# Performance work log

Hardware: AMD Instinct MI355X
Metric: run time of the kernel (lower is better)

Reference implementation:

```python
import jax, jax.numpy as jnp
import numpy as np

N_NODES = 100000
N_EDGES = 1600000
IN_FEATS = 128
N_HIDDEN = 128
N_CLASSES = 16
INIT_EPS = 0.0
N_GIN_LAYERS = 4  # n_layers + 1


def setup_inputs() -> dict:
    key = jax.random.key(0)
    ks = jax.random.split(key, 16)
    features = jax.random.normal(ks[0], (N_NODES, IN_FEATS), dtype=jnp.float32)
    src = jax.random.randint(ks[1], (N_EDGES,), 0, N_NODES, dtype=jnp.int64)
    dst = jax.random.randint(ks[2], (N_EDGES,), 0, N_NODES, dtype=jnp.int64)
    def linear(k, fin, fout):
        bound = 1.0 / np.sqrt(fin)
        kw, kb = jax.random.split(k)
        W = jax.random.uniform(kw, (fin, fout), jnp.float32, -bound, bound)
        b = jax.random.uniform(kb, (fout,), jnp.float32, -bound, bound)
        return W, b
    W0, b0 = linear(ks[3], IN_FEATS, N_HIDDEN)
    W1, b1 = linear(ks[4], N_HIDDEN, N_HIDDEN)
    W2, b2 = linear(ks[5], N_HIDDEN, N_HIDDEN)
    W3, b3 = linear(ks[6], N_HIDDEN, N_CLASSES)
    eps = jnp.full((N_GIN_LAYERS,), INIT_EPS, dtype=jnp.float32)
    return {"features": features, "src": src, "dst": dst,
            "W0": W0, "b0": b0, "W1": W1, "b1": b1,
            "W2": W2, "b2": b2, "W3": W3, "b3": b3, "eps": eps}


def _mean_agg(h, src, dst, inv_deg):
    # gather neighbor features along edges, sum into dst, divide by in-degree
    agg = jax.ops.segment_sum(h[src], dst, num_segments=N_NODES)
    return agg * inv_deg


def _gin_layer(h, src, dst, inv_deg, eps, W, b, relu):
    z = (1.0 + eps) * h + _mean_agg(h, src, dst, inv_deg)
    out = z @ W + b  # Dropout is identity in eval mode
    return jax.nn.relu(out) if relu else out


def reference(features, src, dst, W0, b0, W1, b1, W2, b2, W3, b3, eps):
    deg = jax.ops.segment_sum(jnp.ones((src.shape[0],), features.dtype), dst,
                              num_segments=N_NODES)
    inv_deg = (1.0 / jnp.maximum(deg, 1.0))[:, None]
    h = _gin_layer(features, src, dst, inv_deg, eps[0], W0, b0, relu=True)
    h = _gin_layer(h, src, dst, inv_deg, eps[1], W1, b1, relu=True)
    h = _gin_layer(h, src, dst, inv_deg, eps[2], W2, b2, relu=True)
    h = _gin_layer(h, src, dst, inv_deg, eps[3], W3, b3, relu=False)
    return h
```

## Files before the change

### kernel.cpp

```cpp
#include <hip/hip_runtime.h>

#define NODES 100000
#define EDGES 1600000
#define FEATS 128
#define NCLS  16

#define BSH    6
#define BNODES 64
#define NB     ((NODES + BNODES - 1) / BNODES)
#define CHUNK  8192
#define NBLK   ((EDGES + CHUNK - 1) / CHUNK)
#define NHIST  (NB * NBLK)
#define BCAP   2048
#define NGRP   ((NODES + 15) / 16)

typedef unsigned int  u32;
typedef unsigned short u16;
typedef unsigned long long u64;
typedef __attribute__((ext_vector_type(8))) short short8;
typedef __attribute__((ext_vector_type(4))) float f32x4;

__device__ __forceinline__ float b2f(u16 v){ return __uint_as_float(((u32)v)<<16); }
__device__ __forceinline__ u16 f2b(float f){
  u32 u = __float_as_uint(f);
  u += 0x7fffu + ((u>>16)&1u);
  return (u16)(u>>16);
}
__device__ __forceinline__ float blo(u32 p){ return __uint_as_float(p<<16); }
__device__ __forceinline__ float bhi(u32 p){ return __uint_as_float(p & 0xffff0000u); }

__device__ __forceinline__ void gload16(const u16* g, u16* l){
  __builtin_amdgcn_global_load_lds(
      (const __attribute__((address_space(1))) u32*)g,
      (__attribute__((address_space(3))) u32*)l, 16, 0, 0);
}


__global__ __launch_bounds__(256) void pA_k(const int* __restrict__ dst,
                                            int* __restrict__ gh, int E){
  __shared__ int hist[NB];
  int t = threadIdx.x, blk = blockIdx.x;
  for (int j = t; j < NB; j += 256) hist[j] = 0;
  __syncthreads();
  int e0 = blk*CHUNK, e1 = e0 + CHUNK; if (e1 > E) e1 = E;
  for (int e = e0 + t; e < e1; e += 256) atomicAdd(&hist[dst[e] >> BSH], 1);
  __syncthreads();
  for (int j = t; j < NB; j += 256) gh[j*NBLK + blk] = hist[j];
}


__global__ __launch_bounds__(256) void scan1_k(const int* __restrict__ in, int* __restrict__ out,
                                               int* __restrict__ bsum, int n){
  __shared__ int sh[256];
  int t = threadIdx.x;
  int base = blockIdx.x*2048 + t*8;
  int v[8]; int s = 0;
  #pragma unroll
  for (int j=0;j<8;++j) v[j] = (base+j < n) ? in[base+j] : 0;
  #pragma unroll
  for (int j=0;j<8;++j){ int tmp = v[j]; v[j] = s; s += tmp; }
  sh[t] = s; __syncthreads();
  for (int off=1; off<256; off<<=1){
    int x = (t>=off) ? sh[t-off] : 0;
    __syncthreads();
    sh[t] += x;
    __syncthreads();
  }
  int excl = sh[t] - s;
  #pragma unroll
  for (int j=0;j<8;++j) if (base+j < n) out[base+j] = excl + v[j];
  if (t == 255) bsum[blockIdx.x] = sh[255];
}

__global__ __launch_bounds__(256) void scan2_k(const int* __restrict__ bsum,
                                               int* __restrict__ boff, int nb){
  __shared__ int sh[256];
  int t = threadIdx.x;
  int v = (t < nb) ? bsum[t] : 0;
  sh[t] = v; __syncthreads();
  for (int off=1; off<256; off<<=1){
    int x = (t>=off) ? sh[t-off] : 0;
    __syncthreads();
    sh[t] += x;
    __syncthreads();
  }
  if (t < nb) boff[t] = sh[t] - v;
}

__global__ void scan3_k(int* __restrict__ gscan, const int* __restrict__ boff,
                        int* __restrict__ bstart, int n){
  int i = blockIdx.x*256 + threadIdx.x;
  if (i < n){
    int v = gscan[i] + boff[i>>11];
    gscan[i] = v;
    if (i % NBLK == 0) bstart[i / NBLK] = v;
    if (i == 0) bstart[NB] = EDGES;
  }
}


__global__ __launch_bounds__(256) void pC_k(const int* __restrict__ src,
    const int* __restrict__ dst, const int* __restrict__ gscan,
    u32* __restrict__ elist, int E){
  __shared__ int A[NB];
  __shared__ int B[NB];
  __shared__ int sp[256];
  __shared__ u32 pay[CHUNK];
  __shared__ u16 bkt[CHUNK];
  int t = threadIdx.x, blk = blockIdx.x;
  for (int j = t; j < NB; j += 256) A[j] = 0;
  __syncthreads();
  int e0 = blk*CHUNK, e1 = e0 + CHUNK; if (e1 > E) e1 = E;
  int cnt = e1 - e0;
  for (int e = e0 + t; e < e1; e += 256) atomicAdd(&A[dst[e] >> BSH], 1);
  __syncthreads();
  {
    int base = t*7;
    int cv[7]; int s = 0;
    #pragma unroll
    for (int j=0;j<7;++j){ int idx = base+j; cv[j] = (idx < NB) ? A[idx] : 0; s += cv[j]; }
    sp[t] = s; __syncthreads();
    for (int off=1; off<256; off<<=1){
      int x = (t>=off) ? sp[t-off] : 0;
      __syncthreads();
      sp[t] += x;
      __syncthreads();
    }
    int run = sp[t] - s;
    #pragma unroll
    for (int j=0;j<7;++j){
      int idx = base+j;
      if (idx < NB){ A[idx] = run; B[idx] = run; run += cv[j]; }
    }
  }
  __syncthreads();
  for (int j = t; j < NB; j += 256) A[j] = gscan[j*NBLK + blk] - A[j];
  __syncthreads();
  for (int e = e0 + t; e < e1; e += 256){
    int d = dst[e];
    int b = d >> BSH;
    u32 w = ((u32)(d & (BNODES-1)) << 17) | (u32)src[e];
    int r = atomicAdd(&B[b], 1);
    pay[r] = w; bkt[r] = (u16)b;
  }
  __syncthreads();
  for (int i = t; i < cnt; i += 256){
    int b = bkt[i];
    elist[i + A[b]] = pay[i];
  }
}


__global__ __launch_bounds__(256) void csr_k(u32* __restrict__ elist,
    const int* __restrict__ bstart, int* __restrict__ offs, int* __restrict__ degs,
    float* __restrict__ invd, int M){
  __shared__ int hist[BNODES];
  __shared__ int pos[BNODES];
  __shared__ u32 buf[BCAP];
  __shared__ u32 buf2[BCAP];
  int b = blockIdx.x, t = threadIdx.x;
  if (b == 0 && t == 0) offs[M] = EDGES;
  if (t < BNODES) hist[t] = 0;
  __syncthreads();
  int s0 = bstart[b];
  int cnt = bstart[b+1] - s0; if (cnt > BCAP) cnt = BCAP;
  u32* el = elist + s0;
  for (int e = t; e < cnt; e += 256){
    u32 w = el[e];
    buf[e] = w;
    atomicAdd(&hist[w>>17], 1);
  }
  __syncthreads();
  if (t < BNODES){
    int v = hist[t];
    int s = v;
    for (int off = 1; off < BNODES; off <<= 1){
      int x = __shfl_up(s, off);
      if (t >= off) s += x;
    }
    int excl = s - v;
    pos[t] = excl;
    int node = b*BNODES + t;
    if (node < M){
      offs[node] = s0 + excl;
      degs[node] = v;
      invd[node] = 1.f / fmaxf((float)v, 1.f);
    }
  }
  __syncthreads();
  for (int e = t; e < cnt; e += 256){
    u32 w = buf[e];
    int p = atomicAdd(&pos[w>>17], 1);
    buf2[p] = w;
  }
  __syncthreads();
  for (int e = t; e < cnt; e += 256) el[e] = buf2[e];
}


__global__ void convf_k(const float* __restrict__ in, u16* __restrict__ o, int n4){
  int i = blockIdx.x*256 + threadIdx.x;
  if (i < n4){
    float4 x = ((const float4*)in)[i];
    ushort4 r;
    r.x = f2b(x.x); r.y = f2b(x.y); r.z = f2b(x.z); r.w = f2b(x.w);
    ((ushort4*)o)[i] = r;
  }
}

__global__ void convw_k(const float* __restrict__ W, u16* __restrict__ Wt, int Kd, int Nd){
  int i = blockIdx.x*256 + threadIdx.x;
  if (i < Kd*Nd){
    int k = i / Nd, nn = i - k*Nd;
    Wt[nn*Kd + k] = f2b(W[i]);
  }
}


template<int NT>
__global__ __launch_bounds__(256) void gemm_k(const u16* __restrict__ h,
                                              const u16* __restrict__ Wt,
                                              u16* __restrict__ y, int M){
  const int K = FEATS;
  const int N = NT*16;
  int lane = threadIdx.x & 63;
  int wave = threadIdx.x >> 6;
  int m    = lane & 15;
  int quad = lane >> 4;
  int row0 = (blockIdx.x*4 + wave)*16;
  if (row0 >= M) return;
  int rowA = row0 + m; if (rowA > M-1) rowA = M-1;
  const u16* pa = h + (size_t)rowA*K + quad*8;

  f32x4 acc[NT];
  #pragma unroll
  for (int j=0;j<NT;++j) acc[j] = (f32x4){0.f,0.f,0.f,0.f};

  #pragma unroll
  for (int kk=0; kk<K; kk+=32){
    short8 a = *(const short8*)(pa + kk);
    #pragma unroll
    for (int j=0;j<NT;++j){
      short8 b = *(const short8*)(Wt + (size_t)(j*16 + m)*K + kk + quad*8);
      acc[j] = __builtin_amdgcn_mfma_f32_16x16x32_bf16(a, b, acc[j], 0, 0, 0);
    }
  }

  #pragma unroll
  for (int j=0;j<NT;++j){
    #pragma unroll
    for (int r=0;r<4;++r){
      int row = row0 + quad*4 + r;
      if (row < M) y[(size_t)row*N + j*16 + m] = f2b(acc[j][r]);
    }
  }
}


#define TRRD(dstv, lit) asm volatile("ds_read_b64_tr_b16 %0, %1 offset:" lit \
                                     : "=v"(dstv) : "v"(trb_i))

__global__ __launch_bounds__(256) void aggM_k(const u16* __restrict__ y,
    const u32* __restrict__ el, const int* __restrict__ offs,
    const float* __restrict__ invd, const float* __restrict__ bias,
    const float* __restrict__ epsv, int ei, u16* __restrict__ hout){
  __shared__ __align__(128) u16 ybuf[4][2][4096];
  int lane = threadIdx.x & 63;
  int wave = threadIdx.x >> 6;
  int grp = blockIdx.x*4 + wave;
  if (grp >= NGRP) return;
  int v0 = grp << 4;
  int m    = lane & 15;
  int quad = lane >> 4;
  int li   = lane & 31;
  u32 tgt = (u32)(((grp & 3) << 4) + m);

  u16* lb0 = &ybuf[wave][0][0];
  typedef __attribute__((address_space(3))) u16 lds_u16;
  u32 lbaddr = (u32)(size_t)(lds_u16*)lb0;
  u32 trb0 = lbaddr + (u32)(quad*2048) + (u32)(m*8);

  int rsel = (lane & 7) >> 1;
  int gcol = ((lane >> 3) << 4) + ((lane & 1) << 3);

  int e0 = offs[v0];
  int e1 = offs[v0 + 16];
  int nstep = (e1 - e0 + 31) >> 5;

  f32x4 acc[8];
  #pragma unroll
  for (int cb=0;cb<8;++cb) acc[cb] = (f32x4){0.f,0.f,0.f,0.f};

  auto elp = [&](int st)->const u32*{
    int idx = e0 + (st<<5) + li;
    if (idx > EDGES-1) idx = EDGES-1;
    return el + idx;
  };
  auto maskw = [&](u32 v, int st)->u32{
    int idx = e0 + (st<<5) + li;
    return (idx < e1) ? v : 0xFFFE0000u;
  };
  auto gathers = [&](u32 wm, u16* dstbuf){
    #pragma unroll
    for (int i=0;i<8;++i){
      u32 ws = (u32)__shfl((int)wm, 4*i + rsel);
      int srow = (int)(ws & 0x1FFFFu);
      gload16(y + ((size_t)srow << 7) + gcol, dstbuf + i*512);
    }
  };

  u32 v0w;
  asm volatile("global_load_dword %0, %1, off" : "=v"(v0w) : "v"(elp(0)));
  asm volatile("s_waitcnt vmcnt(0)" : "+v"(v0w) :: "memory");
  u32 wcur = maskw(v0w, 0);
  u32 vnext;
  asm volatile("global_load_dword %0, %1, off" : "=v"(vnext) : "v"(elp(1)));
  gathers(wcur, lb0);

  for (int st = 0; st < nstep; ++st){
    asm volatile("s_waitcnt vmcnt(8)" : "+v"(vnext) :: "memory");
    u32 wn = maskw(vnext, st+1);
    u32 vfut;
    asm volatile("global_load_dword %0, %1, off" : "=v"(vfut) : "v"(elp(st+2)));
    gathers(wn, lb0 + (((st+1)&1) << 12));

    union { u32 wv[4]; short8 s; } au;
    #pragma unroll
    for (int p=0;p<4;++p){
      u32 w0 = (u32)__shfl((int)wcur, quad*8 + 2*p);
      u32 w1 = (u32)__shfl((int)wcur, quad*8 + 2*p + 1);
      au.wv[p] = (((w0>>17) == tgt) ? 0x3F80u : 0u)
               | (((w1>>17) == tgt) ? 0x3F800000u : 0u);
    }

    asm volatile("s_waitcnt vmcnt(9)" ::: "memory");
    __builtin_amdgcn_sched_barrier(0);

    u32 trb_i = trb0 + (u32)((st&1) << 13);
    u64 t[16];
    TRRD(t[0],  "0");    TRRD(t[1],  "1024");
    TRRD(t[2],  "128");  TRRD(t[3],  "1152");
    TRRD(t[4],  "256");  TRRD(t[5],  "1280");
    TRRD(t[6],  "384");  TRRD(t[7],  "1408");
    TRRD(t[8],  "512");  TRRD(t[9],  "1536");
    TRRD(t[10], "640");  TRRD(t[11], "1664");
    TRRD(t[12], "768");  TRRD(t[13], "1792");
    TRRD(t[14], "896");  TRRD(t[15], "1920");
    asm volatile("s_waitcnt lgkmcnt(0)" ::: "memory");
    __builtin_amdgcn_sched_barrier(0);

    #pragma unroll
    for (int cb=0;cb<8;++cb){
      union { u64 d[2]; short8 s; } bu;
      bu.d[0] = t[2*cb]; bu.d[1] = t[2*cb+1];
      acc[cb] = __builtin_amdgcn_mfma_f32_16x16x32_bf16(au.s, bu.s, acc[cb], 0, 0, 0);
    }

    wcur = wn; vnext = vfut;
  }
  asm volatile("s_waitcnt vmcnt(0)" ::: "memory");

  float myinv = invd[v0 + m];
  float invr[4];
  #pragma unroll
  for (int r=0;r<4;++r) invr[r] = __shfl(myinv, quad*4 + r);
  float e1s = 1.f + epsv[ei];
  #pragma unroll
  for (int cb=0;cb<8;++cb){
    float bi = bias[cb*16 + m];
    #pragma unroll
    for (int r=0;r<4;++r){
      size_t off = (size_t)(v0 + quad*4 + r)*FEATS + cb*16 + m;
      float self = b2f(y[off]);
      float o = fmaxf(e1s*self + invr[r]*acc[cb][r] + bi, 0.f);
      hout[off] = f2b(o);
    }
  }
}


__global__ __launch_bounds__(256) void aggF2_k(const u16* __restrict__ y,
    const u32* __restrict__ el, const int* __restrict__ offs,
    const int* __restrict__ degs, const float* __restrict__ invd,
    const float* __restrict__ bias, const float* __restrict__ epsv,
    float* __restrict__ out, int M){
  int lane = threadIdx.x & 63;
  int v = blockIdx.x*4 + (threadIdx.x >> 6);
  if (v >= M) return;
  int sub = lane >> 3;
  int f2  = lane & 7;
  const u32* y2 = (const u32*)y;
  int start = offs[v], deg = degs[v];
  float acc0 = 0.f, acc1 = 0.f;
  for (int e = sub; e < deg; e += 8){
    u32 s = el[start + e] & 0x1FFFFu;
    u32 p = y2[(size_t)s*8 + f2];
    acc0 += blo(p); acc1 += bhi(p);
  }
  acc0 += __shfl_xor(acc0, 8);  acc1 += __shfl_xor(acc1, 8);
  acc0 += __shfl_xor(acc0, 16); acc1 += __shfl_xor(acc1, 16);
  acc0 += __shfl_xor(acc0, 32); acc1 += __shfl_xor(acc1, 32);
  if (sub == 0){
    u32 pv = y2[(size_t)v*8 + f2];
    float2 bi = ((const float2*)bias)[f2];
    float e1s = 1.f + epsv[3];
    float inv = invd[v];
    out[(size_t)v*NCLS + 2*f2    ] = e1s*blo(pv) + inv*acc0 + bi.x;
    out[(size_t)v*NCLS + 2*f2 + 1] = e1s*bhi(pv) + inv*acc1 + bi.y;
  }
}


extern "C" void kernel_launch(void* const* d_in, const int* in_sizes, int n_in,
                              void* d_out, int out_size, void* d_ws, size_t ws_size,
                              hipStream_t stream){
  const float* feats = (const float*)d_in[0];
  const int*   src   = (const int*)d_in[1];
  const int*   dst   = (const int*)d_in[2];
  const float* W0 = (const float*)d_in[3];  const float* b0 = (const float*)d_in[4];
  const float* W1 = (const float*)d_in[5];  const float* b1 = (const float*)d_in[6];
  const float* W2 = (const float*)d_in[7];  const float* b2 = (const float*)d_in[8];
  const float* W3 = (const float*)d_in[9];  const float* b3 = (const float*)d_in[10];
  const float* eps = (const float*)d_in[11];

  char* w = (char*)d_ws;
  auto alloc = [&](size_t bytes)->char*{
    char* p = w; w += (bytes + 255) & ~(size_t)255; return p;
  };
  int*  gh    = (int*)alloc(sizeof(int)*NHIST);
  int*  gscan = (int*)alloc(sizeof(int)*NHIST);
  int*  bsum  = (int*)alloc(sizeof(int)*256);
  int*  boff  = (int*)alloc(sizeof(int)*256);
  int*  bstart= (int*)alloc(sizeof(int)*(NB+1));
  int*  offs  = (int*)alloc(sizeof(int)*(NODES+1));
  int*  degs  = (int*)alloc(sizeof(int)*NODES);
  float* invd = (float*)alloc(sizeof(float)*NODES);
  u32*  elist = (u32*)alloc(sizeof(u32)*EDGES);
  u16*  hb    = (u16*)alloc(sizeof(u16)*(size_t)NODES*FEATS);
  u16*  yb    = (u16*)alloc(sizeof(u16)*(size_t)NODES*FEATS);
  u16*  Wt0   = (u16*)alloc(sizeof(u16)*128*128);
  u16*  Wt1   = (u16*)alloc(sizeof(u16)*128*128);
  u16*  Wt2   = (u16*)alloc(sizeof(u16)*128*128);
  u16*  Wt3   = (u16*)alloc(sizeof(u16)*16*128);

  pA_k<<<NBLK, 256, 0, stream>>>(dst, gh, EDGES);
  int snb = (NHIST + 2047)/2048;
  scan1_k<<<snb, 256, 0, stream>>>(gh, gscan, bsum, NHIST);
  scan2_k<<<1, 256, 0, stream>>>(bsum, boff, snb);
  scan3_k<<<(NHIST+255)/256, 256, 0, stream>>>(gscan, boff, bstart, NHIST);
  pC_k<<<NBLK, 256, 0, stream>>>(src, dst, gscan, elist, EDGES);
  csr_k<<<NB, 256, 0, stream>>>(elist, bstart, offs, degs, invd, NODES);

  convf_k<<<((NODES*FEATS/4)+255)/256, 256, 0, stream>>>(feats, hb, NODES*FEATS/4);
  convw_k<<<(128*128+255)/256, 256, 0, stream>>>(W0, Wt0, 128, 128);
  convw_k<<<(128*128+255)/256, 256, 0, stream>>>(W1, Wt1, 128, 128);
  convw_k<<<(128*128+255)/256, 256, 0, stream>>>(W2, Wt2, 128, 128);
  convw_k<<<(128*16 +255)/256, 256, 0, stream>>>(W3, Wt3, 128, 16);

  int gblocks = (NODES + 63)/64;
  int mblocks = (NGRP + 3)/4;
  int ablocks = (NODES + 3)/4;

  gemm_k<8><<<gblocks, 256, 0, stream>>>(hb, Wt0, yb, NODES);
  aggM_k<<<mblocks, 256, 0, stream>>>(yb, elist, offs, invd, b0, eps, 0, hb);
  gemm_k<8><<<gblocks, 256, 0, stream>>>(hb, Wt1, yb, NODES);
  aggM_k<<<mblocks, 256, 0, stream>>>(yb, elist, offs, invd, b1, eps, 1, hb);
  gemm_k<8><<<gblocks, 256, 0, stream>>>(hb, Wt2, yb, NODES);
  aggM_k<<<mblocks, 256, 0, stream>>>(yb, elist, offs, invd, b2, eps, 2, hb);

  gemm_k<1><<<gblocks, 256, 0, stream>>>(hb, Wt3, yb, NODES);
  aggF2_k<<<ablocks, 256, 0, stream>>>(yb, elist, offs, degs, invd, b3, eps, (float*)d_out, NODES);
}
```

Before: 499.2 us.

## Fuse next-layer GEMM into aggregation kernel epilogue

```diff
diff --git a/kernel.cpp b/kernel.cpp
--- a/kernel.cpp
+++ b/kernel.cpp
@@ -260,10 +260,13 @@
 #define TRRD(dstv, lit) asm volatile("ds_read_b64_tr_b16 %0, %1 offset:" lit \
                                      : "=v"(dstv) : "v"(trb_i))
 
-__global__ __launch_bounds__(256) void aggM_k(const u16* __restrict__ y,
+template<int NTO>
+__global__ __launch_bounds__(256) void fagg_k(const u16* __restrict__ y,
     const u32* __restrict__ el, const int* __restrict__ offs,
     const float* __restrict__ invd, const float* __restrict__ bias,
-    const float* __restrict__ epsv, int ei, u16* __restrict__ hout){
+    const float* __restrict__ epsv, int ei,
+    const u16* __restrict__ Wn,
+    u16* __restrict__ yout){
   __shared__ __align__(128) u16 ybuf[4][2][4096];
   int lane = threadIdx.x & 63;
   int wave = threadIdx.x >> 6;
@@ -365,6 +368,7 @@
   #pragma unroll
   for (int r=0;r<4;++r) invr[r] = __shfl(myinv, quad*4 + r);
   float e1s = 1.f + epsv[ei];
+  u16* zl = lb0;
   #pragma unroll
   for (int cb=0;cb<8;++cb){
     float bi = bias[cb*16 + m];
@@ -372,9 +376,27 @@
     for (int r=0;r<4;++r){
       size_t off = (size_t)(v0 + quad*4 + r)*FEATS + cb*16 + m;
       float self = b2f(y[off]);
-      float o = fmaxf(e1s*self + invr[r]*acc[cb][r] + bi, 0.f);
-      hout[off] = f2b(o);
-    }
+      float h = fmaxf(e1s*self + invr[r]*acc[cb][r] + bi, 0.f);
+      zl[(quad*4 + r)*136 + cb*16 + m] = f2b(h);
+    }
+  }
+
+  short8 af[4];
+  #pragma unroll
+  for (int kb=0;kb<4;++kb)
+    af[kb] = *(const short8*)(zl + m*136 + kb*32 + quad*8);
+
+  #pragma unroll
+  for (int nb=0;nb<NTO;++nb){
+    f32x4 a2 = (f32x4){0.f,0.f,0.f,0.f};
+    #pragma unroll
+    for (int kb=0;kb<4;++kb){
+      short8 bf = *(const short8*)(Wn + (size_t)(nb*16 + m)*FEATS + kb*32 + quad*8);
+      a2 = __builtin_amdgcn_mfma_f32_16x16x32_bf16(af[kb], bf, a2, 0, 0, 0);
+    }
+    #pragma unroll
+    for (int r=0;r<4;++r)
+      yout[(size_t)(v0 + quad*4 + r)*(NTO*16) + nb*16 + m] = f2b(a2[r]);
   }
 }
 
@@ -462,12 +484,8 @@
   int ablocks = (NODES + 3)/4;
 
   gemm_k<8><<<gblocks, 256, 0, stream>>>(hb, Wt0, yb, NODES);
-  aggM_k<<<mblocks, 256, 0, stream>>>(yb, elist, offs, invd, b0, eps, 0, hb);
-  gemm_k<8><<<gblocks, 256, 0, stream>>>(hb, Wt1, yb, NODES);
-  aggM_k<<<mblocks, 256, 0, stream>>>(yb, elist, offs, invd, b1, eps, 1, hb);
-  gemm_k<8><<<gblocks, 256, 0, stream>>>(hb, Wt2, yb, NODES);
-  aggM_k<<<mblocks, 256, 0, stream>>>(yb, elist, offs, invd, b2, eps, 2, hb);
-
-  gemm_k<1><<<gblocks, 256, 0, stream>>>(hb, Wt3, yb, NODES);
-  aggF2_k<<<ablocks, 256, 0, stream>>>(yb, elist, offs, degs, invd, b3, eps, (float*)d_out, NODES);
-}
+  fagg_k<8><<<mblocks, 256, 0, stream>>>(yb, elist, offs, invd, b0, eps, 0, Wt1, hb);
+  fagg_k<8><<<mblocks, 256, 0, stream>>>(hb, elist, offs, invd, b1, eps, 1, Wt2, yb);
+  fagg_k<1><<<mblocks, 256, 0, stream>>>(yb, elist, offs, invd, b2, eps, 2, Wt3, hb);
+  aggF2_k<<<ablocks, 256, 0, stream>>>(hb, elist, offs, degs, invd, b3, eps, (float*)d_out, NODES);
+}
```

Result: faster. 456.9 us (-8.5%).
